# Kernel optimization log

Measured on AMD Instinct MI355X. Metric: run time of the kernel, lower is better.

The kernel has to match this reference:

```python
import jax, jax.numpy as jnp
import numpy as np

B, N, T, ET = 256, 256, 100, 4
MSG_HID, MSG_OUT, N_HID, N_CLASSES = 128, 64, 64, 2
N_EDGES = N * (N - 1) // 2  # 32640


def _xavier(k, out_dim, in_dim):
    std = (2.0 / (in_dim + out_dim)) ** 0.5
    return jax.random.normal(k, (out_dim, in_dim), dtype=jnp.float32) * std


def setup_inputs() -> dict:
    key = jax.random.key(0)
    ks = jax.random.split(key, 7)
    return {
        "inputs": jax.random.normal(ks[0], (B, N, T), dtype=jnp.float32),
        "sparse_edges": jax.random.uniform(ks[1], (B, N_EDGES, ET), dtype=jnp.float32),
        "w1": _xavier(ks[2], MSG_HID, N), "b1": jnp.full((MSG_HID,), 0.1, jnp.float32),
        "w2": _xavier(ks[3], MSG_OUT, MSG_HID), "b2": jnp.full((MSG_OUT,), 0.1, jnp.float32),
        "wo1": _xavier(ks[4], N_HID, MSG_OUT), "bo1": jnp.full((N_HID,), 0.1, jnp.float32),
        "wo2": _xavier(ks[5], N_HID, N_HID), "bo2": jnp.full((N_HID,), 0.1, jnp.float32),
        "wo3": _xavier(ks[6], N_CLASSES, N_HID), "bo3": jnp.full((N_CLASSES,), 0.1, jnp.float32),
    }


def reference(inputs, sparse_edges, w1, b1, w2, b2, wo1, bo1, wo2, bo2, wo3, bo3):
    b, n, _ = inputs.shape
    r, c = np.triu_indices(n, k=1)  # static index pattern
    # Scatter all non-null edge types at once: [B, ET-1, N, N]
    se = jnp.swapaxes(sparse_edges[:, :, 1:], 1, 2)  # [B, ET-1, E]
    adj = jnp.zeros((b, se.shape[1], n, n), dtype=se.dtype)
    adj = adj.at[:, :, r, c].set(se)
    adj = adj + jnp.swapaxes(adj, -1, -2)  # symmetrize
    # Message MLP (dropout_prob = 0 -> identity)
    h = jax.nn.relu(jnp.einsum('beij,hj->beih', adj, w1) + b1)   # [B,ET-1,N,msg_hid]
    m = jax.nn.relu(jnp.einsum('beih,oh->beio', h, w2) + b2)     # [B,ET-1,N,msg_out]
    # Weighted sum over edge types: weight for type i is i*0.2, i=1..ET-1
    wts = (jnp.arange(1, sparse_edges.shape[2]) * 0.2).astype(m.dtype)
    out = jnp.einsum('beio,e->bio', m, wts)                      # [B,N,msg_out]
    # Output head
    p = jax.nn.relu(out @ wo1.T + bo1)
    p = jax.nn.relu(p @ wo2.T + bo2)
    p = jnp.mean(p, axis=1)  # mean over atoms
    return p @ wo3.T + bo3   # [B, n_classes]
```

## Files before the change

kernel.cpp:

```cpp
#include <hip/hip_runtime.h>

#define N_   256
#define E_   32640

typedef __bf16 bf16x8 __attribute__((ext_vector_type(8)));
typedef unsigned short u16x8 __attribute__((ext_vector_type(8)));
typedef float f32x4 __attribute__((ext_vector_type(4)));

__device__ __forceinline__ unsigned short cvt_bf16(float f) {
  unsigned u = __float_as_uint(f);
  u = (u + 0x7FFFu + ((u >> 16) & 1u)) >> 16;
  return (unsigned short)u;
}

__device__ __forceinline__ bf16x8 ldfrag(const unsigned short* base, int row, int kbyte, int rowbytes) {
  int byte = (row * rowbytes + kbyte) ^ ((row & 7) << 4);
  return *reinterpret_cast<const bf16x8*>(reinterpret_cast<const char*>(base) + byte);
}

__device__ __forceinline__ void st2(unsigned short* base, int row, int colbyte, int rowbytes, unsigned short v) {
  int byte = (row * rowbytes + colbyte) ^ ((row & 7) << 4);
  *reinterpret_cast<unsigned short*>(reinterpret_cast<char*>(base) + byte) = v;
}

__device__ __forceinline__ bf16x8 pack8(float4 lo, float4 hi) {
  u16x8 u;
  u[0] = cvt_bf16(lo.x); u[1] = cvt_bf16(lo.y); u[2] = cvt_bf16(lo.z); u[3] = cvt_bf16(lo.w);
  u[4] = cvt_bf16(hi.x); u[5] = cvt_bf16(hi.y); u[6] = cvt_bf16(hi.z); u[7] = cvt_bf16(hi.w);
  return __builtin_bit_cast(bf16x8, u);
}

__global__ __launch_bounds__(1024, 4) void mlpdec_kernel(
    const float* __restrict__ se_g,
    const float* __restrict__ w1,  const float* __restrict__ b1,
    const float* __restrict__ w2,  const float* __restrict__ b2,
    const float* __restrict__ wo1, const float* __restrict__ bo1,
    const float* __restrict__ wo2, const float* __restrict__ bo2,
    const float* __restrict__ wo3, const float* __restrict__ bo3,
    float* __restrict__ out)
{
  __shared__ __align__(16) unsigned short sA[3][64 * N_];
  __shared__ __align__(16) unsigned short sH[64 * 128];
  __shared__ __align__(16) unsigned short sWO1[64 * 64];
  __shared__ __align__(16) unsigned short sWO2[64 * 64];
  __shared__ float sB1[128], sB2[64], sBO1[64], sBO2[64], sWo3[128], sBo3[2];
  __shared__ float sAccW[16][64];
  __shared__ float sMean[64];

  const int tid = threadIdx.x;
  const int b   = blockIdx.x;
  const int w   = tid >> 6;
  const int l   = tid & 63;
  const int l15 = l & 15;
  const int lk  = l >> 4;
  const int kb0 = lk * 16;

  const int c1 = w & 7;
  const int rb = w >> 3;
  const int c2 = w & 3;
  const int r2 = w >> 2;

  bf16x8 W1f[8];
  {
    const float* p = w1 + (c1 * 16 + l15) * 256 + lk * 8;
    #pragma unroll
    for (int ks = 0; ks < 8; ++ks) {
      float4 lo = *reinterpret_cast<const float4*>(p + ks * 32);
      float4 hi = *reinterpret_cast<const float4*>(p + ks * 32 + 4);
      W1f[ks] = pack8(lo, hi);
    }
  }
  bf16x8 W2f[4];
  {
    const float* p = w2 + (c2 * 16 + l15) * 128 + lk * 8;
    #pragma unroll
    for (int ks = 0; ks < 4; ++ks) {
      float4 lo = *reinterpret_cast<const float4*>(p + ks * 32);
      float4 hi = *reinterpret_cast<const float4*>(p + ks * 32 + 4);
      W2f[ks] = pack8(lo, hi);
    }
  }

  {
    int t = tid;
    int idx = t << 2;
    {
      const float4 v = *reinterpret_cast<const float4*>(wo1 + idx);
      int row = idx >> 6;
      ushort4 u = make_ushort4(cvt_bf16(v.x), cvt_bf16(v.y), cvt_bf16(v.z), cvt_bf16(v.w));
      int byte = (idx * 2) ^ ((row & 7) << 4);
      *reinterpret_cast<ushort4*>(reinterpret_cast<char*>(sWO1) + byte) = u;
    }
    {
      const float4 v = *reinterpret_cast<const float4*>(wo2 + idx);
      int row = idx >> 6;
      ushort4 u = make_ushort4(cvt_bf16(v.x), cvt_bf16(v.y), cvt_bf16(v.z), cvt_bf16(v.w));
      int byte = (idx * 2) ^ ((row & 7) << 4);
      *reinterpret_cast<ushort4*>(reinterpret_cast<char*>(sWO2) + byte) = u;
    }
  }
  if (tid < 128) sB1[tid] = b1[tid];
  if (tid < 64)  { sB2[tid] = b2[tid]; sBO1[tid] = bo1[tid]; sBO2[tid] = bo2[tid]; }
  if (tid < 128) sWo3[tid] = wo3[tid];
  if (tid < 2)   sBo3[tid] = bo3[tid];
  reinterpret_cast<float*>(sAccW)[tid] = 0.f;
  __syncthreads();

  const float4* seB = reinterpret_cast<const float4*>(se_g) + (size_t)b * E_;
  unsigned short* sX = sH;
  unsigned short* sP = sH + 64 * 64;

  for (int r0 = 0; r0 < N_; r0 += 64) {
    #pragma unroll
    for (int rr = 0; rr < 4; ++rr) {
      int lr = (w << 2) + rr;
      int gi = r0 + lr;
      int cnt = 255 - gi;
      int ubase = gi * 255 - ((gi * (gi - 1)) >> 1);
      for (int jj = l; jj < cnt; jj += 64) {
        float4 v = seB[ubase + jj];
        int cb = (gi + 1 + jj) * 2;
        st2(sA[0], lr, cb, 512, cvt_bf16(v.y));
        st2(sA[1], lr, cb, 512, cvt_bf16(v.z));
        st2(sA[2], lr, cb, 512, cvt_bf16(v.w));
      }
    }
    for (int j = w; j < r0 + 63; j += 16) {
      int i0  = (j + 1 > r0) ? (j + 1) : r0;
      int cnt = r0 + 64 - i0;
      if (l < cnt) {
        int i = i0 + l;
        int u = j * 255 - ((j * (j - 1)) >> 1) + (i - j - 1);
        float4 v = seB[u];
        int lr = i - r0, cb = j * 2;
        st2(sA[0], lr, cb, 512, cvt_bf16(v.y));
        st2(sA[1], lr, cb, 512, cvt_bf16(v.z));
        st2(sA[2], lr, cb, 512, cvt_bf16(v.w));
      }
    }
    if (tid < 64) {
      int cb = (r0 + tid) * 2;
      st2(sA[0], tid, cb, 512, 0);
      st2(sA[1], tid, cb, 512, 0);
      st2(sA[2], tid, cb, 512, 0);
    }
    __syncthreads();

    f32x4 outAcc = {0.f, 0.f, 0.f, 0.f};

    for (int e = 0; e < 3; ++e) {
      {
        f32x4 acc0 = {0,0,0,0}, acc1 = {0,0,0,0};
        const unsigned short* sAe = sA[e];
        int arow0 = rb * 16 + l15;
        int arow1 = (rb + 2) * 16 + l15;
        #pragma unroll
        for (int ks = 0; ks < 8; ++ks) {
          int kb = ks * 64 + kb0;
          bf16x8 a0 = ldfrag(sAe, arow0, kb, 512);
          bf16x8 a1 = ldfrag(sAe, arow1, kb, 512);
          acc0 = __builtin_amdgcn_mfma_f32_16x16x32_bf16(a0, W1f[ks], acc0, 0, 0, 0);
          acc1 = __builtin_amdgcn_mfma_f32_16x16x32_bf16(a1, W1f[ks], acc1, 0, 0, 0);
        }
        int cc = c1 * 16 + l15;
        float bias = sB1[cc];
        #pragma unroll
        for (int r = 0; r < 4; ++r) {
          st2(sH, rb * 16 + lk * 4 + r,       cc * 2, 256, cvt_bf16(fmaxf(acc0[r] + bias, 0.f)));
          st2(sH, (rb + 2) * 16 + lk * 4 + r, cc * 2, 256, cvt_bf16(fmaxf(acc1[r] + bias, 0.f)));
        }
      }
      __syncthreads();
      {
        f32x4 acc = {0,0,0,0};
        int arow = r2 * 16 + l15;
        #pragma unroll
        for (int ks = 0; ks < 4; ++ks) {
          bf16x8 a = ldfrag(sH, arow, ks * 64 + kb0, 256);
          acc = __builtin_amdgcn_mfma_f32_16x16x32_bf16(a, W2f[ks], acc, 0, 0, 0);
        }
        float bias = sB2[c2 * 16 + l15];
        float wte  = 0.2f * (float)(e + 1);
        #pragma unroll
        for (int r = 0; r < 4; ++r)
          outAcc[r] += wte * fmaxf(acc[r] + bias, 0.f);
      }
      __syncthreads();
    }

    {
      int col = c2 * 16 + l15;
      #pragma unroll
      for (int r = 0; r < 4; ++r)
        st2(sX, r2 * 16 + lk * 4 + r, col * 2, 128, cvt_bf16(outAcc[r]));
    }
    __syncthreads();
    {
      f32x4 acc = {0,0,0,0};
      int arow = r2 * 16 + l15;
      int brow = c2 * 16 + l15;
      #pragma unroll
      for (int ks = 0; ks < 2; ++ks) {
        bf16x8 a  = ldfrag(sX,   arow, ks * 64 + kb0, 128);
        bf16x8 bb = ldfrag(sWO1, brow, ks * 64 + kb0, 128);
        acc = __builtin_amdgcn_mfma_f32_16x16x32_bf16(a, bb, acc, 0, 0, 0);
      }
      float bias = sBO1[c2 * 16 + l15];
      #pragma unroll
      for (int r = 0; r < 4; ++r)
        st2(sP, r2 * 16 + lk * 4 + r, (c2 * 16 + l15) * 2, 128, cvt_bf16(fmaxf(acc[r] + bias, 0.f)));
    }
    __syncthreads();
    {
      f32x4 acc = {0,0,0,0};
      int arow = r2 * 16 + l15;
      int brow = c2 * 16 + l15;
      #pragma unroll
      for (int ks = 0; ks < 2; ++ks) {
        bf16x8 a  = ldfrag(sP,   arow, ks * 64 + kb0, 128);
        bf16x8 bb = ldfrag(sWO2, brow, ks * 64 + kb0, 128);
        acc = __builtin_amdgcn_mfma_f32_16x16x32_bf16(a, bb, acc, 0, 0, 0);
      }
      float bias = sBO2[c2 * 16 + l15];
      float s = 0.f;
      #pragma unroll
      for (int r = 0; r < 4; ++r) s += fmaxf(acc[r] + bias, 0.f);
      s += __shfl_xor(s, 16);
      s += __shfl_xor(s, 32);
      if (lk == 0) sAccW[w][c2 * 16 + l15] += s;
    }
    __syncthreads();
  }

  if (tid < 64) {
    float s = 0.f;
    #pragma unroll
    for (int ww = 0; ww < 16; ++ww) s += sAccW[ww][tid];
    sMean[tid] = s * (1.0f / 256.0f);
  }
  __syncthreads();
  if (tid < 128) {
    int c = tid >> 6;
    float v = sMean[l] * sWo3[c * 64 + l];
    #pragma unroll
    for (int off = 32; off > 0; off >>= 1) v += __shfl_down(v, off);
    if (l == 0) out[b * 2 + c] = v + sBo3[c];
  }
}

extern "C" void kernel_launch(void* const* d_in, const int* in_sizes, int n_in,
                              void* d_out, int out_size, void* d_ws, size_t ws_size,
                              hipStream_t stream) {
  (void)in_sizes; (void)n_in; (void)d_ws; (void)ws_size; (void)out_size;
  const float* se  = (const float*)d_in[1];
  const float* w1  = (const float*)d_in[2];
  const float* b1  = (const float*)d_in[3];
  const float* w2  = (const float*)d_in[4];
  const float* b2  = (const float*)d_in[5];
  const float* wo1 = (const float*)d_in[6];
  const float* bo1 = (const float*)d_in[7];
  const float* wo2 = (const float*)d_in[8];
  const float* bo2 = (const float*)d_in[9];
  const float* wo3 = (const float*)d_in[10];
  const float* bo3 = (const float*)d_in[11];
  mlpdec_kernel<<<dim3(256), dim3(1024), 0, stream>>>(
      se, w1, b1, w2, b2, wo1, bo1, wo2, bo2, wo3, bo3, (float*)d_out);
}
```

Baseline: 101.2 us.

## Split each batch into 32-row chunks across blocks with a separate finish kernel

The per-batch 1024-thread block that looped over four 64-row slices becomes 2048 blocks of 512 threads, each handling one 32-row chunk of one batch. Per-chunk column sums go to a workspace buffer, and a small second kernel reduces them, takes the mean and applies the final linear layer. The aim is more parallelism and smaller LDS per block so more blocks can be resident and overlap loads with compute. In exchange, the W1 and W2 fragments and the output-head weights are loaded and converted eight times per batch, and there is an extra kernel launch. Block indices are remapped so that neighbouring blocks take different batches.

```diff
diff --git a/kernel.cpp b/kernel.cpp
--- a/kernel.cpp
+++ b/kernel.cpp
@@ -1,7 +1,7 @@
 #include <hip/hip_runtime.h>
 
-#define N_   256
-#define E_   32640
+#define N_ 256
+#define E_ 32640
 
 typedef __bf16 bf16x8 __attribute__((ext_vector_type(8)));
 typedef unsigned short u16x8 __attribute__((ext_vector_type(8)));
@@ -30,35 +30,36 @@
   return __builtin_bit_cast(bf16x8, u);
 }
 
-__global__ __launch_bounds__(1024, 4) void mlpdec_kernel(
+__global__ __launch_bounds__(512, 4) void chunk_kernel(
     const float* __restrict__ se_g,
     const float* __restrict__ w1,  const float* __restrict__ b1,
     const float* __restrict__ w2,  const float* __restrict__ b2,
     const float* __restrict__ wo1, const float* __restrict__ bo1,
     const float* __restrict__ wo2, const float* __restrict__ bo2,
-    const float* __restrict__ wo3, const float* __restrict__ bo3,
-    float* __restrict__ out)
+    float* __restrict__ ws)
 {
-  __shared__ __align__(16) unsigned short sA[3][64 * N_];
-  __shared__ __align__(16) unsigned short sH[64 * 128];
+  __shared__ __align__(16) unsigned short sA[3][32 * N_];
+  __shared__ __align__(16) unsigned short sH[32 * 128];
   __shared__ __align__(16) unsigned short sWO1[64 * 64];
   __shared__ __align__(16) unsigned short sWO2[64 * 64];
-  __shared__ float sB1[128], sB2[64], sBO1[64], sBO2[64], sWo3[128], sBo3[2];
-  __shared__ float sAccW[16][64];
-  __shared__ float sMean[64];
+  __shared__ float sB1[128], sB2[64], sBO1[64], sBO2[64];
+  __shared__ float sAccW[8][64];
 
   const int tid = threadIdx.x;
-  const int b   = blockIdx.x;
+  const int i   = blockIdx.x;
+  const int batch = (i & 7) * 32 + ((i >> 3) & 31);
+  const int chunk = i >> 8;
+  const int r0    = chunk * 32;
+
   const int w   = tid >> 6;
   const int l   = tid & 63;
   const int l15 = l & 15;
   const int lk  = l >> 4;
   const int kb0 = lk * 16;
 
-  const int c1 = w & 7;
-  const int rb = w >> 3;
+  const int c1 = w;
+  const int r2 = w >> 2;
   const int c2 = w & 3;
-  const int r2 = w >> 2;
 
   bf16x8 W1f[8];
   {
@@ -81,177 +82,186 @@
     }
   }
 
-  {
-    int t = tid;
+  for (int t = tid; t < 1024; t += 512) {
     int idx = t << 2;
+    int row = idx >> 6;
+    int byte = (idx * 2) ^ ((row & 7) << 4);
     {
       const float4 v = *reinterpret_cast<const float4*>(wo1 + idx);
-      int row = idx >> 6;
       ushort4 u = make_ushort4(cvt_bf16(v.x), cvt_bf16(v.y), cvt_bf16(v.z), cvt_bf16(v.w));
-      int byte = (idx * 2) ^ ((row & 7) << 4);
       *reinterpret_cast<ushort4*>(reinterpret_cast<char*>(sWO1) + byte) = u;
     }
     {
       const float4 v = *reinterpret_cast<const float4*>(wo2 + idx);
-      int row = idx >> 6;
       ushort4 u = make_ushort4(cvt_bf16(v.x), cvt_bf16(v.y), cvt_bf16(v.z), cvt_bf16(v.w));
-      int byte = (idx * 2) ^ ((row & 7) << 4);
       *reinterpret_cast<ushort4*>(reinterpret_cast<char*>(sWO2) + byte) = u;
     }
   }
   if (tid < 128) sB1[tid] = b1[tid];
   if (tid < 64)  { sB2[tid] = b2[tid]; sBO1[tid] = bo1[tid]; sBO2[tid] = bo2[tid]; }
-  if (tid < 128) sWo3[tid] = wo3[tid];
-  if (tid < 2)   sBo3[tid] = bo3[tid];
   reinterpret_cast<float*>(sAccW)[tid] = 0.f;
-  __syncthreads();
-
-  const float4* seB = reinterpret_cast<const float4*>(se_g) + (size_t)b * E_;
+
+  const float4* seB = reinterpret_cast<const float4*>(se_g) + (size_t)batch * E_;
   unsigned short* sX = sH;
-  unsigned short* sP = sH + 64 * 64;
-
-  for (int r0 = 0; r0 < N_; r0 += 64) {
-    #pragma unroll
-    for (int rr = 0; rr < 4; ++rr) {
-      int lr = (w << 2) + rr;
-      int gi = r0 + lr;
-      int cnt = 255 - gi;
-      int ubase = gi * 255 - ((gi * (gi - 1)) >> 1);
-      for (int jj = l; jj < cnt; jj += 64) {
-        float4 v = seB[ubase + jj];
-        int cb = (gi + 1 + jj) * 2;
+  unsigned short* sP = sH + 32 * 64;
+
+  #pragma unroll
+  for (int rr = 0; rr < 4; ++rr) {
+    int lr = (w << 2) + rr;
+    int gi = r0 + lr;
+    int cnt = 255 - gi;
+    int ubase = gi * 255 - ((gi * (gi - 1)) >> 1);
+    for (int jj = l; jj < cnt; jj += 64) {
+      float4 v = seB[ubase + jj];
+      int cb = (gi + 1 + jj) * 2;
+      st2(sA[0], lr, cb, 512, cvt_bf16(v.y));
+      st2(sA[1], lr, cb, 512, cvt_bf16(v.z));
+      st2(sA[2], lr, cb, 512, cvt_bf16(v.w));
+    }
+  }
+  {
+    int sub = tid >> 5, l32 = tid & 31;
+    for (int j = sub; j < r0 + 31; j += 16) {
+      int i0  = (j + 1 > r0) ? (j + 1) : r0;
+      int cnt = r0 + 32 - i0;
+      if (l32 < cnt) {
+        int ii = i0 + l32;
+        int u = j * 255 - ((j * (j - 1)) >> 1) + (ii - j - 1);
+        float4 v = seB[u];
+        int lr = ii - r0, cb = j * 2;
         st2(sA[0], lr, cb, 512, cvt_bf16(v.y));
         st2(sA[1], lr, cb, 512, cvt_bf16(v.z));
         st2(sA[2], lr, cb, 512, cvt_bf16(v.w));
       }
     }
-    for (int j = w; j < r0 + 63; j += 16) {
-      int i0  = (j + 1 > r0) ? (j + 1) : r0;
-      int cnt = r0 + 64 - i0;
-      if (l < cnt) {
-        int i = i0 + l;
-        int u = j * 255 - ((j * (j - 1)) >> 1) + (i - j - 1);
-        float4 v = seB[u];
-        int lr = i - r0, cb = j * 2;
-        st2(sA[0], lr, cb, 512, cvt_bf16(v.y));
-        st2(sA[1], lr, cb, 512, cvt_bf16(v.z));
-        st2(sA[2], lr, cb, 512, cvt_bf16(v.w));
-      }
-    }
-    if (tid < 64) {
-      int cb = (r0 + tid) * 2;
-      st2(sA[0], tid, cb, 512, 0);
-      st2(sA[1], tid, cb, 512, 0);
-      st2(sA[2], tid, cb, 512, 0);
-    }
-    __syncthreads();
-
-    f32x4 outAcc = {0.f, 0.f, 0.f, 0.f};
-
-    for (int e = 0; e < 3; ++e) {
-      {
-        f32x4 acc0 = {0,0,0,0}, acc1 = {0,0,0,0};
-        const unsigned short* sAe = sA[e];
-        int arow0 = rb * 16 + l15;
-        int arow1 = (rb + 2) * 16 + l15;
-        #pragma unroll
-        for (int ks = 0; ks < 8; ++ks) {
-          int kb = ks * 64 + kb0;
-          bf16x8 a0 = ldfrag(sAe, arow0, kb, 512);
-          bf16x8 a1 = ldfrag(sAe, arow1, kb, 512);
-          acc0 = __builtin_amdgcn_mfma_f32_16x16x32_bf16(a0, W1f[ks], acc0, 0, 0, 0);
-          acc1 = __builtin_amdgcn_mfma_f32_16x16x32_bf16(a1, W1f[ks], acc1, 0, 0, 0);
-        }
-        int cc = c1 * 16 + l15;
-        float bias = sB1[cc];
-        #pragma unroll
-        for (int r = 0; r < 4; ++r) {
-          st2(sH, rb * 16 + lk * 4 + r,       cc * 2, 256, cvt_bf16(fmaxf(acc0[r] + bias, 0.f)));
-          st2(sH, (rb + 2) * 16 + lk * 4 + r, cc * 2, 256, cvt_bf16(fmaxf(acc1[r] + bias, 0.f)));
-        }
-      }
-      __syncthreads();
-      {
-        f32x4 acc = {0,0,0,0};
-        int arow = r2 * 16 + l15;
-        #pragma unroll
-        for (int ks = 0; ks < 4; ++ks) {
-          bf16x8 a = ldfrag(sH, arow, ks * 64 + kb0, 256);
-          acc = __builtin_amdgcn_mfma_f32_16x16x32_bf16(a, W2f[ks], acc, 0, 0, 0);
-        }
-        float bias = sB2[c2 * 16 + l15];
-        float wte  = 0.2f * (float)(e + 1);
-        #pragma unroll
-        for (int r = 0; r < 4; ++r)
-          outAcc[r] += wte * fmaxf(acc[r] + bias, 0.f);
-      }
-      __syncthreads();
-    }
-
-    {
-      int col = c2 * 16 + l15;
-      #pragma unroll
-      for (int r = 0; r < 4; ++r)
-        st2(sX, r2 * 16 + lk * 4 + r, col * 2, 128, cvt_bf16(outAcc[r]));
+  }
+  if (tid < 32) {
+    int cb = (r0 + tid) * 2;
+    st2(sA[0], tid, cb, 512, 0);
+    st2(sA[1], tid, cb, 512, 0);
+    st2(sA[2], tid, cb, 512, 0);
+  }
+  __syncthreads();
+
+  f32x4 outAcc = {0.f, 0.f, 0.f, 0.f};
+
+  for (int e = 0; e < 3; ++e) {
+    {
+      f32x4 acc0 = {0,0,0,0}, acc1 = {0,0,0,0};
+      const unsigned short* sAe = sA[e];
+      #pragma unroll
+      for (int ks = 0; ks < 8; ++ks) {
+        int kb = ks * 64 + kb0;
+        bf16x8 a0 = ldfrag(sAe, l15,      kb, 512);
+        bf16x8 a1 = ldfrag(sAe, 16 + l15, kb, 512);
+        acc0 = __builtin_amdgcn_mfma_f32_16x16x32_bf16(a0, W1f[ks], acc0, 0, 0, 0);
+        acc1 = __builtin_amdgcn_mfma_f32_16x16x32_bf16(a1, W1f[ks], acc1, 0, 0, 0);
+      }
+      int cc = c1 * 16 + l15;
+      float bias = sB1[cc];
+      #pragma unroll
+      for (int r = 0; r < 4; ++r) {
+        st2(sH, lk * 4 + r,      cc * 2, 256, cvt_bf16(fmaxf(acc0[r] + bias, 0.f)));
+        st2(sH, 16 + lk * 4 + r, cc * 2, 256, cvt_bf16(fmaxf(acc1[r] + bias, 0.f)));
+      }
     }
     __syncthreads();
     {
       f32x4 acc = {0,0,0,0};
       int arow = r2 * 16 + l15;
-      int brow = c2 * 16 + l15;
-      #pragma unroll
-      for (int ks = 0; ks < 2; ++ks) {
-        bf16x8 a  = ldfrag(sX,   arow, ks * 64 + kb0, 128);
-        bf16x8 bb = ldfrag(sWO1, brow, ks * 64 + kb0, 128);
-        acc = __builtin_amdgcn_mfma_f32_16x16x32_bf16(a, bb, acc, 0, 0, 0);
-      }
-      float bias = sBO1[c2 * 16 + l15];
+      #pragma unroll
+      for (int ks = 0; ks < 4; ++ks) {
+        bf16x8 a = ldfrag(sH, arow, ks * 64 + kb0, 256);
+        acc = __builtin_amdgcn_mfma_f32_16x16x32_bf16(a, W2f[ks], acc, 0, 0, 0);
+      }
+      float bias = sB2[c2 * 16 + l15];
+      float wte  = 0.2f * (float)(e + 1);
       #pragma unroll
       for (int r = 0; r < 4; ++r)
-        st2(sP, r2 * 16 + lk * 4 + r, (c2 * 16 + l15) * 2, 128, cvt_bf16(fmaxf(acc[r] + bias, 0.f)));
+        outAcc[r] += wte * fmaxf(acc[r] + bias, 0.f);
     }
     __syncthreads();
-    {
-      f32x4 acc = {0,0,0,0};
-      int arow = r2 * 16 + l15;
-      int brow = c2 * 16 + l15;
-      #pragma unroll
-      for (int ks = 0; ks < 2; ++ks) {
-        bf16x8 a  = ldfrag(sP,   arow, ks * 64 + kb0, 128);
-        bf16x8 bb = ldfrag(sWO2, brow, ks * 64 + kb0, 128);
-        acc = __builtin_amdgcn_mfma_f32_16x16x32_bf16(a, bb, acc, 0, 0, 0);
-      }
-      float bias = sBO2[c2 * 16 + l15];
-      float s = 0.f;
-      #pragma unroll
-      for (int r = 0; r < 4; ++r) s += fmaxf(acc[r] + bias, 0.f);
-      s += __shfl_xor(s, 16);
-      s += __shfl_xor(s, 32);
-      if (lk == 0) sAccW[w][c2 * 16 + l15] += s;
-    }
-    __syncthreads();
-  }
+  }
+
+  {
+    int col = c2 * 16 + l15;
+    #pragma unroll
+    for (int r = 0; r < 4; ++r)
+      st2(sX, r2 * 16 + lk * 4 + r, col * 2, 128, cvt_bf16(outAcc[r]));
+  }
+  __syncthreads();
+  {
+    f32x4 acc = {0,0,0,0};
+    int arow = r2 * 16 + l15;
+    int brow = c2 * 16 + l15;
+    #pragma unroll
+    for (int ks = 0; ks < 2; ++ks) {
+      bf16x8 a  = ldfrag(sX,   arow, ks * 64 + kb0, 128);
+      bf16x8 bb = ldfrag(sWO1, brow, ks * 64 + kb0, 128);
+      acc = __builtin_amdgcn_mfma_f32_16x16x32_bf16(a, bb, acc, 0, 0, 0);
+    }
+    float bias = sBO1[c2 * 16 + l15];
+    #pragma unroll
+    for (int r = 0; r < 4; ++r)
+      st2(sP, r2 * 16 + lk * 4 + r, (c2 * 16 + l15) * 2, 128, cvt_bf16(fmaxf(acc[r] + bias, 0.f)));
+  }
+  __syncthreads();
+  {
+    f32x4 acc = {0,0,0,0};
+    int arow = r2 * 16 + l15;
+    int brow = c2 * 16 + l15;
+    #pragma unroll
+    for (int ks = 0; ks < 2; ++ks) {
+      bf16x8 a  = ldfrag(sP,   arow, ks * 64 + kb0, 128);
+      bf16x8 bb = ldfrag(sWO2, brow, ks * 64 + kb0, 128);
+      acc = __builtin_amdgcn_mfma_f32_16x16x32_bf16(a, bb, acc, 0, 0, 0);
+    }
+    float bias = sBO2[c2 * 16 + l15];
+    float s = 0.f;
+    #pragma unroll
+    for (int r = 0; r < 4; ++r) s += fmaxf(acc[r] + bias, 0.f);
+    s += __shfl_xor(s, 16);
+    s += __shfl_xor(s, 32);
+    if (lk == 0) sAccW[w][c2 * 16 + l15] = s;
+  }
+  __syncthreads();
 
   if (tid < 64) {
     float s = 0.f;
     #pragma unroll
-    for (int ww = 0; ww < 16; ++ww) s += sAccW[ww][tid];
-    sMean[tid] = s * (1.0f / 256.0f);
-  }
-  __syncthreads();
-  if (tid < 128) {
-    int c = tid >> 6;
-    float v = sMean[l] * sWo3[c * 64 + l];
-    #pragma unroll
-    for (int off = 32; off > 0; off >>= 1) v += __shfl_down(v, off);
-    if (l == 0) out[b * 2 + c] = v + sBo3[c];
+    for (int ww = 0; ww < 8; ++ww) s += sAccW[ww][tid];
+    ws[((size_t)batch * 8 + chunk) * 64 + tid] = s;
+  }
+}
+
+__global__ __launch_bounds__(64) void finish_kernel(
+    const float* __restrict__ ws,
+    const float* __restrict__ wo3, const float* __restrict__ bo3,
+    float* __restrict__ out)
+{
+  int b = blockIdx.x;
+  int l = threadIdx.x;
+  float s = 0.f;
+  #pragma unroll
+  for (int c = 0; c < 8; ++c) s += ws[((size_t)b * 8 + c) * 64 + l];
+  s *= (1.0f / 256.0f);
+  float v0 = s * wo3[l];
+  float v1 = s * wo3[64 + l];
+  #pragma unroll
+  for (int off = 32; off > 0; off >>= 1) {
+    v0 += __shfl_down(v0, off);
+    v1 += __shfl_down(v1, off);
+  }
+  if (l == 0) {
+    out[b * 2 + 0] = v0 + bo3[0];
+    out[b * 2 + 1] = v1 + bo3[1];
   }
 }
 
 extern "C" void kernel_launch(void* const* d_in, const int* in_sizes, int n_in,
                               void* d_out, int out_size, void* d_ws, size_t ws_size,
                               hipStream_t stream) {
-  (void)in_sizes; (void)n_in; (void)d_ws; (void)ws_size; (void)out_size;
+  (void)in_sizes; (void)n_in; (void)ws_size; (void)out_size;
   const float* se  = (const float*)d_in[1];
   const float* w1  = (const float*)d_in[2];
   const float* b1  = (const float*)d_in[3];
@@ -263,6 +273,8 @@
   const float* bo2 = (const float*)d_in[9];
   const float* wo3 = (const float*)d_in[10];
   const float* bo3 = (const float*)d_in[11];
-  mlpdec_kernel<<<dim3(256), dim3(1024), 0, stream>>>(
-      se, w1, b1, w2, b2, wo1, bo1, wo2, bo2, wo3, bo3, (float*)d_out);
-}
+  float* ws = (float*)d_ws;
+  chunk_kernel<<<dim3(2048), dim3(512), 0, stream>>>(
+      se, w1, b1, w2, b2, wo1, bo1, wo2, bo2, ws);
+  finish_kernel<<<dim3(256), dim3(64), 0, stream>>>(ws, wo3, bo3, (float*)d_out);
+}
```

New measurement: 105.2 us. 1.04x slower.
